# Kernel optimization log

Hardware: AMD Instinct MI355X
Metric: run time of the kernel (lower is better)

Reference implementation:

```python
import jax, jax.numpy as jnp
import numpy as np

D = 1024
N_HEAD = 16
D_HEAD = D // N_HEAD
B, S = 4, 2048
EPS = 1e-6


def rmsnorm(x, w):
    # x: [..., d_head]
    return x / jnp.sqrt(jnp.mean(x * x, axis=-1, keepdims=True) + EPS) * w


def setup_inputs() -> dict:
    key = jax.random.key(0)
    ks = jax.random.split(key, 6)
    x = jax.random.normal(ks[0], (B, S, D), dtype=jnp.float32)
    # causal mask: True means masked (upper triangle above diagonal)
    mask = jnp.triu(jnp.ones((S, S), dtype=bool), k=1)
    scale = 1.0 / np.sqrt(D)
    W_qkv = jax.random.normal(ks[1], (D, 3 * D), dtype=jnp.float32) * scale
    b_qkv = jnp.zeros((3 * D,), dtype=jnp.float32)
    W_o = jax.random.normal(ks[2], (D, D), dtype=jnp.float32) * scale
    b_o = jnp.zeros((D,), dtype=jnp.float32)
    wq = jnp.ones((D_HEAD,), dtype=jnp.float32)
    wk = jnp.ones((D_HEAD,), dtype=jnp.float32)
    return {"x": x, "mask": mask, "W_qkv": W_qkv, "b_qkv": b_qkv,
            "W_o": W_o, "b_o": b_o, "wq": wq, "wk": wk}


def reference(x, mask, W_qkv, b_qkv, W_o, b_o, wq, wk):
    b, s, d = x.shape
    qkv = x @ W_qkv + b_qkv  # [b,s,3d]
    q, k, v = jnp.split(qkv, 3, axis=-1)
    q = q.reshape(b, s, N_HEAD, D_HEAD)
    k = k.reshape(b, s, N_HEAD, D_HEAD)
    v = v.reshape(b, s, N_HEAD, D_HEAD)
    q = rmsnorm(q, wq)
    k = rmsnorm(k, wk)
    # NOTE: no 1/sqrt(d_head) scaling, faithful to the source
    attn = jnp.einsum('bqhd,bkhd->bhqk', q, k)
    attn = jnp.where(mask[None, None, :, :], -jnp.inf, attn)
    attn = jax.nn.softmax(attn, axis=-1)
    z = jnp.einsum('bhqk,bkhd->bqhd', attn, v).reshape(b, s, d)
    return z @ W_o + b_o
```

## Files before the change

kernel.cpp:

```cpp
#include <hip/hip_runtime.h>
#include <cmath>

typedef _Float16 half_t;
typedef _Float16 half8 __attribute__((ext_vector_type(8)));
typedef _Float16 half4v __attribute__((ext_vector_type(4)));
typedef float float4v __attribute__((ext_vector_type(4)));

#define LOG2E 1.44269504088896340736f

#define GLDS16(g, l)                                                                   \
    __builtin_amdgcn_global_load_lds((const __attribute__((address_space(1))) void*)(g), \
                                     (__attribute__((address_space(3))) void*)(l), 16, 0, 0)

#define BAR_LGKM() __asm__ volatile("s_waitcnt lgkmcnt(0)\n\ts_barrier" ::: "memory")
#define BAR_VM(n)  __asm__ volatile("s_waitcnt vmcnt(" #n ")\n\ts_barrier" ::: "memory")

__global__ void cast_f32_f16(const float* __restrict__ in, half_t* __restrict__ out, int n) {
    int i = (blockIdx.x * blockDim.x + threadIdx.x) * 4;
    if (i >= n) return;
    float4 v = *(const float4*)(in + i);
    half4v o;
    o[0] = (half_t)v.x; o[1] = (half_t)v.y; o[2] = (half_t)v.z; o[3] = (half_t)v.w;
    *(half4v*)(out + i) = o;
}

__global__ void transpose_cast(const float* __restrict__ in, half_t* __restrict__ out, int R, int C) {
    __shared__ float tile[32][33];
    int c0 = blockIdx.x * 32, r0 = blockIdx.y * 32;
    int tx = threadIdx.x, ty = threadIdx.y;
    for (int p = 0; p < 4; p++) {
        int r = r0 + ty + p * 8;
        tile[ty + p * 8][tx] = in[(size_t)r * C + c0 + tx];
    }
    __syncthreads();
    for (int p = 0; p < 4; p++) {
        int c = c0 + ty + p * 8;
        out[(size_t)c * R + r0 + tx] = (half_t)tile[tx][ty + p * 8];
    }
}

template <int MODE>
__global__ __launch_bounds__(256, 3) void gemm_f16(
    const half_t* __restrict__ A,
    const half_t* __restrict__ Bt,
    const float* __restrict__ bias,
    void* __restrict__ Cout,
    int M, int N, int K,
    const float* __restrict__ wq, const float* __restrict__ wk,
    half_t* __restrict__ Qh, half_t* __restrict__ Kh)
{
    __shared__ __align__(16) half_t As[3][128 * 32];
    __shared__ __align__(16) half_t Bs[3][128 * 32];
    int t = threadIdx.x;
    int lane = t & 63, w = t >> 6;
    int m0 = blockIdx.x * 128, n0 = blockIdx.y * 128;
    int wm = (w >> 1) * 64, wn = (w & 1) * 64;
    int lrow = lane & 15, quad = lane >> 4;

    int lc = ((t & 3) - (t >> 3)) & 3;
    const half_t* gA = A  + (size_t)(m0 + (t >> 2)) * K + lc * 8;
    const half_t* gB = Bt + (size_t)(n0 + (t >> 2)) * K + lc * 8;
    half_t* ldsA[3] = { &As[0][w * 512], &As[1][w * 512], &As[2][w * 512] };
    half_t* ldsB[3] = { &Bs[0][w * 512], &Bs[1][w * 512], &Bs[2][w * 512] };

    int posq = (quad + (lrow >> 1)) & 3;

    float4v acc[4][4] = {};

    GLDS16(gA,                       ldsA[0]);
    GLDS16(gA + (size_t)64 * K,      ldsA[0] + 2048);
    GLDS16(gB,                       ldsB[0]);
    GLDS16(gB + (size_t)64 * K,      ldsB[0] + 2048);
    GLDS16(gA + 32,                  ldsA[1]);
    GLDS16(gA + (size_t)64 * K + 32, ldsA[1] + 2048);
    GLDS16(gB + 32,                  ldsB[1]);
    GLDS16(gB + (size_t)64 * K + 32, ldsB[1] + 2048);

    int nk = K >> 5;
    for (int ki = 0; ki < nk; ki++) {
        int cur = ki % 3, pre = (ki + 2) % 3;
        BAR_LGKM();
        if (ki + 2 < nk) {
            int kp = (ki + 2) << 5;
            GLDS16(gA + kp,                  ldsA[pre]);
            GLDS16(gA + (size_t)64 * K + kp, ldsA[pre] + 2048);
            GLDS16(gB + kp,                  ldsB[pre]);
            GLDS16(gB + (size_t)64 * K + kp, ldsB[pre] + 2048);
            BAR_VM(8);
        } else if (ki + 1 < nk) {
            BAR_VM(4);
        } else {
            BAR_VM(0);
        }
        half8 af[4], bf[4];
        for (int i = 0; i < 4; i++) af[i] = *(const half8*)(&As[cur][(wm + i * 16 + lrow) * 32 + posq * 8]);
        for (int i = 0; i < 4; i++) bf[i] = *(const half8*)(&Bs[cur][(wn + i * 16 + lrow) * 32 + posq * 8]);
        for (int mi = 0; mi < 4; mi++)
            for (int ni = 0; ni < 4; ni++)
                acc[mi][ni] = __builtin_amdgcn_mfma_f32_16x16x32_f16(af[mi], bf[ni], acc[mi][ni], 0, 0, 0);
    }

    if (MODE == 0) {
        float* out = (float*)Cout;
        for (int mi = 0; mi < 4; mi++)
            for (int ni = 0; ni < 4; ni++)
                for (int r = 0; r < 4; r++) {
                    int gr = m0 + wm + mi * 16 + quad * 4 + r;
                    int gc = n0 + wn + ni * 16 + lrow;
                    out[(size_t)gr * N + gc] = acc[mi][ni][r] + bias[gc];
                }
    } else {
        int nglob = n0 + wn;
        if (nglob < 2048) {
            int isK = nglob >> 10;
            int h = (nglob >> 6) & 15;
            const float* wv = isK ? wk : wq;
            half_t* dst = isK ? Kh : Qh;
            float post = isK ? 1.0f : LOG2E;
            for (int mi = 0; mi < 4; mi++)
                for (int r = 0; r < 4; r++) {
                    int gr = m0 + wm + mi * 16 + quad * 4 + r;
                    float v[4]; float ss = 0.f;
                    for (int ni = 0; ni < 4; ni++) {
                        v[ni] = acc[mi][ni][r] + bias[nglob + ni * 16 + lrow];
                        ss += v[ni] * v[ni];
                    }
                    ss += __shfl_xor(ss, 1);
                    ss += __shfl_xor(ss, 2);
                    ss += __shfl_xor(ss, 4);
                    ss += __shfl_xor(ss, 8);
                    float rr = rsqrtf(ss * (1.0f / 64.0f) + 1e-6f) * post;
                    int bb = gr >> 11, s = gr & 2047;
                    size_t rowbase = ((size_t)((bb * 16 + h) * 2048 + s)) * 64;
                    for (int ni = 0; ni < 4; ni++) {
                        int d = ni * 16 + lrow;
                        dst[rowbase + d] = (half_t)(v[ni] * rr * wv[d]);
                    }
                }
        } else {
            half_t* Vt = (half_t*)Cout;
            for (int mi = 0; mi < 4; mi++) {
                int gr = m0 + wm + mi * 16 + quad * 4;
                int bb = gr >> 11, s = gr & 2047;
                for (int ni = 0; ni < 4; ni++) {
                    int dg = nglob + ni * 16 + lrow - 2048;
                    float bv = bias[nglob + ni * 16 + lrow];
                    half4v oh;
                    for (int r = 0; r < 4; r++) oh[r] = (half_t)(acc[mi][ni][r] + bv);
                    *(half4v*)(Vt + ((size_t)((bb * 16 + (dg >> 6)) * 64 + (dg & 63))) * 2048 + s) = oh;
                }
            }
        }
    }
}

__global__ __launch_bounds__(512, 4) void attn(
    const half_t* __restrict__ Qh, const half_t* __restrict__ Kh, const half_t* __restrict__ Vt,
    half_t* __restrict__ Z)
{
    __shared__ __align__(16) half_t Ks[2][128 * 64];
    __shared__ __align__(16) half_t Vs[2][64 * 128];
    __shared__ __align__(16) half_t Ps[8][16 * 64];

    int bh = blockIdx.x;
    int b = bh >> 4, h = bh & 15;
    int t = threadIdx.x, lane = t & 63, w = t >> 6;
    int lrow = lane & 15, quad = lane >> 4;

    int scc = (lane & 7) ^ ((lane >> 3) & 7);
    const half_t* gK0 = Kh + ((size_t)bh * 2048 + w * 16 + (lane >> 3)) * 64 + scc * 8;
    int vr0 = w * 8 + (lane >> 4);
    int vc0 = (lane & 15) ^ (lane >> 4);
    int vc1 = (lane & 15) ^ ((lane >> 4) + 4);
    const half_t* gV0 = Vt + ((size_t)bh * 64 + vr0) * 2048 + vc0 * 8;
    const half_t* gV1 = Vt + ((size_t)bh * 64 + vr0 + 4) * 2048 + vc1 * 8;
    half_t* ldsK[2] = { &Ks[0][w * 1024], &Ks[1][w * 1024] };
    half_t* ldsV[2] = { &Vs[0][w * 1024], &Vs[1][w * 1024] };

    int sw = lrow & 7;
    int cA = (quad ^ sw) * 8;
    int cB = ((quad + 4) ^ sw) * 8;
    half_t* PsW = &Ps[w][lrow * 64];

    for (int pass = 0; pass < 2; pass++) {
        int qt = pass ? (15 - (int)blockIdx.y) : (int)blockIdx.y;
        int q0w = qt * 128 + w * 16;

        const half_t* Qbase = Qh + ((size_t)bh * 2048 + q0w + lrow) * 64;
        half8 qf0 = *(const half8*)(Qbase + quad * 8);
        half8 qf1 = *(const half8*)(Qbase + 32 + quad * 8);

        float4v ot[4] = {};
        float m = -__builtin_inff(), l = 0.f;

        int nt = qt + 1;
        __syncthreads();
        GLDS16(gK0,       ldsK[0]);
        GLDS16(gK0 + 512, ldsK[0] + 512);
        GLDS16(gV0,       ldsV[0]);
        GLDS16(gV1,       ldsV[0] + 512);

        for (int kt = 0; kt < nt; kt++) {
            int cur = kt & 1, nxt = cur ^ 1;
            int kb = kt * 128;
            BAR_LGKM();
            if (kt + 1 < nt) {
                size_t ko = (size_t)(kb + 128);
                GLDS16(gK0 + ko * 64,       ldsK[nxt]);
                GLDS16(gK0 + ko * 64 + 512, ldsK[nxt] + 512);
                GLDS16(gV0 + ko,            ldsV[nxt]);
                GLDS16(gV1 + ko,            ldsV[nxt] + 512);
                BAR_VM(4);
            } else {
                BAR_VM(0);
            }

            float4v st[8];
            for (int f = 0; f < 8; f++) {
                float4v z = {};
                const half_t* kr = &Ks[cur][(f * 16 + lrow) * 64];
                half8 k0 = *(const half8*)(kr + cA);
                half8 k1 = *(const half8*)(kr + cB);
                z = __builtin_amdgcn_mfma_f32_16x16x32_f16(k0, qf0, z, 0, 0, 0);
                z = __builtin_amdgcn_mfma_f32_16x16x32_f16(k1, qf1, z, 0, 0, 0);
                st[f] = z;
            }
            if (kb + 127 > q0w) {
                int qabs = q0w + lrow;
                for (int f = 0; f < 8; f++)
                    for (int r = 0; r < 4; r++) {
                        int key = kb + f * 16 + quad * 4 + r;
                        if (key > qabs) st[f][r] = -__builtin_inff();
                    }
            }
            float tm = st[0][0];
            for (int f = 0; f < 8; f++)
                for (int r = 0; r < 4; r++) tm = fmaxf(tm, st[f][r]);
            tm = fmaxf(tm, __shfl_xor(tm, 16));
            tm = fmaxf(tm, __shfl_xor(tm, 32));
            float mn = fmaxf(m, tm);
            float alpha = __builtin_amdgcn_exp2f(m - mn);
            m = mn;
            float rs = 0.f;
            uint2 pw1[4];
            for (int f = 0; f < 8; f++) {
                float p0 = __builtin_amdgcn_exp2f(st[f][0] - mn);
                float p1 = __builtin_amdgcn_exp2f(st[f][1] - mn);
                float p2 = __builtin_amdgcn_exp2f(st[f][2] - mn);
                float p3 = __builtin_amdgcn_exp2f(st[f][3] - mn);
                rs += (p0 + p1) + (p2 + p3);
                uint2 pw;
                pw.x = __builtin_bit_cast(unsigned, __builtin_amdgcn_cvt_pkrtz(p0, p1));
                pw.y = __builtin_bit_cast(unsigned, __builtin_amdgcn_cvt_pkrtz(p2, p3));
                if (f < 4) {
                    int cc = (2 * f + (quad >> 1)) ^ sw;
                    *(uint2*)(PsW + cc * 8 + (quad & 1) * 4) = pw;
                } else {
                    pw1[f - 4] = pw;
                }
            }
            rs += __shfl_xor(rs, 16);
            rs += __shfl_xor(rs, 32);
            l = l * alpha + rs;
            for (int f2 = 0; f2 < 4; f2++)
                for (int r = 0; r < 4; r++) ot[f2][r] *= alpha;

            __asm__ volatile("s_waitcnt lgkmcnt(0)" ::: "memory");
            half8 p0v = *(const half8*)(PsW + cA);
            half8 p1v = *(const half8*)(PsW + cB);
            for (int f2 = 0; f2 < 4; f2++) {
                int row = f2 * 16 + lrow;
                half8 v0 = *(const half8*)(&Vs[cur][row * 128 + ((quad ^ sw)) * 8]);
                half8 v1 = *(const half8*)(&Vs[cur][row * 128 + (((4 + quad) ^ sw)) * 8]);
                ot[f2] = __builtin_amdgcn_mfma_f32_16x16x32_f16(v0, p0v, ot[f2], 0, 0, 0);
                ot[f2] = __builtin_amdgcn_mfma_f32_16x16x32_f16(v1, p1v, ot[f2], 0, 0, 0);
            }
            for (int f = 0; f < 4; f++) {
                int cc = (2 * f + (quad >> 1)) ^ sw;
                *(uint2*)(PsW + cc * 8 + (quad & 1) * 4) = pw1[f];
            }
            __asm__ volatile("s_waitcnt lgkmcnt(0)" ::: "memory");
            half8 p2v = *(const half8*)(PsW + cA);
            half8 p3v = *(const half8*)(PsW + cB);
            for (int f2 = 0; f2 < 4; f2++) {
                int row = f2 * 16 + lrow;
                half8 v2 = *(const half8*)(&Vs[cur][row * 128 + (((8 + quad) ^ sw)) * 8]);
                half8 v3 = *(const half8*)(&Vs[cur][row * 128 + (((12 + quad) ^ sw)) * 8]);
                ot[f2] = __builtin_amdgcn_mfma_f32_16x16x32_f16(v2, p2v, ot[f2], 0, 0, 0);
                ot[f2] = __builtin_amdgcn_mfma_f32_16x16x32_f16(v3, p3v, ot[f2], 0, 0, 0);
            }
        }

        float inv = 1.0f / l;
        size_t base = ((size_t)(b * 2048) + q0w + lrow) * 1024 + h * 64;
        for (int f2 = 0; f2 < 4; f2++) {
            half4v oh;
            for (int r = 0; r < 4; r++) oh[r] = (half_t)(ot[f2][r] * inv);
            *(half4v*)(Z + base + f2 * 16 + quad * 4) = oh;
        }
    }
}

extern "C" void kernel_launch(void* const* d_in, const int* in_sizes, int n_in,
                              void* d_out, int out_size, void* d_ws, size_t ws_size,
                              hipStream_t stream)
{
    const float* x     = (const float*)d_in[0];
    const float* W_qkv = (const float*)d_in[2];
    const float* b_qkv = (const float*)d_in[3];
    const float* W_o   = (const float*)d_in[4];
    const float* b_o   = (const float*)d_in[5];
    const float* wq    = (const float*)d_in[6];
    const float* wk    = (const float*)d_in[7];
    float* out = (float*)d_out;

    char* ws = (char*)d_ws;
    half_t* xh   = (half_t*)(ws);
    half_t* Wqt  = (half_t*)(ws + (16ull << 20));
    half_t* Wot  = (half_t*)(ws + (22ull << 20));
    half_t* Qh   = (half_t*)(ws + (40ull << 20));
    half_t* Kh   = (half_t*)(ws + (56ull << 20));
    half_t* Vt   = (half_t*)(ws + (72ull << 20));
    half_t* zh   = xh;

    cast_f32_f16<<<8192, 256, 0, stream>>>(x, xh, 8192 * 1024);
    transpose_cast<<<dim3(96, 32), dim3(32, 8), 0, stream>>>(W_qkv, Wqt, 1024, 3072);
    transpose_cast<<<dim3(32, 32), dim3(32, 8), 0, stream>>>(W_o, Wot, 1024, 1024);
    gemm_f16<1><<<dim3(64, 24), 256, 0, stream>>>(xh, Wqt, b_qkv, Vt, 8192, 3072, 1024,
                                                  wq, wk, Qh, Kh);
    attn<<<dim3(64, 8), 512, 0, stream>>>(Qh, Kh, Vt, zh);
    gemm_f16<0><<<dim3(64, 8), 256, 0, stream>>>(zh, Wot, b_o, out, 8192, 1024, 1024,
                                                 nullptr, nullptr, nullptr, nullptr);
}
```

Baseline: 270.2 us.

## Add 256x256 ping-pong QKV GEMM with XCD-aware block remap and fused RMSNorm epilogue

```diff
diff --git a/kernel.cpp b/kernel.cpp
--- a/kernel.cpp
+++ b/kernel.cpp
@@ -37,6 +37,192 @@
         int c = c0 + ty + p * 8;
         out[(size_t)c * R + r0 + tx] = (half_t)tile[tx][ty + p * 8];
     }
+}
+
+__global__ __launch_bounds__(512, 2) void gemm_qkv(
+    const half_t* __restrict__ A,
+    const half_t* __restrict__ Bt,
+    const float* __restrict__ bias,
+    const float* __restrict__ wq, const float* __restrict__ wk,
+    half_t* __restrict__ Qh, half_t* __restrict__ Kh, half_t* __restrict__ Vt,
+    int M, int N, int K)
+{
+    __shared__ __align__(16) half_t As[2][2][128 * 64];
+    __shared__ __align__(16) half_t Bs[2][2][256 * 32];
+
+    int t = threadIdx.x;
+    int lane = t & 63, w = t >> 6;
+    int lrow = lane & 15, quad = lane >> 4;
+    int wm = w >> 2, wn = w & 3;
+
+    int cpx = gridDim.x >> 3;
+    int bid = blockIdx.x;
+    int wg = (bid & 7) * cpx + (bid >> 3);
+    int nbn = N >> 8;
+    int mb = wg / nbn, nb = wg % nbn;
+    int m0 = mb << 8, n0 = nb << 8;
+
+    int ar = t >> 3;
+    int ac = (t & 7) ^ (ar & 7);
+    const half_t* gAbase = A + (size_t)(m0 + ar) * K + ac * 8;
+    int br = t >> 2;
+    int bc = t & 3;
+    const half_t* gBbase = Bt + (size_t)(n0 + br) * K + bc * 8;
+
+    auto stageA = [&](int buf, int a, int T) {
+        const half_t* s = gAbase + (size_t)a * 128 * K + T * 64;
+        GLDS16(s,                  &As[buf][a][w * 512]);
+        GLDS16(s + (size_t)64 * K, &As[buf][a][4096 + w * 512]);
+    };
+    auto stageB = [&](int buf, int kh, int T) {
+        const half_t* s = gBbase + T * 64 + kh * 32;
+        GLDS16(s,                   &Bs[buf][kh][w * 512]);
+        GLDS16(s + (size_t)128 * K, &Bs[buf][kh][4096 + w * 512]);
+    };
+
+    int sw = lrow & 7;
+    int cx0 = ((0 + quad) ^ sw) * 8;
+    int cx1 = ((4 + quad) ^ sw) * 8;
+    int aoffs = (wm * 64 + lrow) * 64;
+    int boffs = (wn * 64 + lrow) * 32 + quad * 8;
+
+    half8 af[4][2];
+    half8 b0[4], b1[4];
+    float4v acc[2][4][4] = {};
+
+    auto loadA = [&](int buf, int a) {
+        #pragma unroll
+        for (int mi = 0; mi < 4; mi++) {
+            af[mi][0] = *(const half8*)(&As[buf][a][aoffs + mi * 1024 + cx0]);
+            af[mi][1] = *(const half8*)(&As[buf][a][aoffs + mi * 1024 + cx1]);
+        }
+    };
+    auto loadB = [&](int buf, int kh, half8* bf) {
+        #pragma unroll
+        for (int ni = 0; ni < 4; ni++)
+            bf[ni] = *(const half8*)(&Bs[buf][kh][boffs + ni * 512]);
+    };
+
+#define PHASE_OPEN()                                               \
+    do {                                                           \
+        __asm__ volatile("s_barrier" ::: "memory");                \
+        __asm__ volatile("s_waitcnt lgkmcnt(0)" ::: "memory");     \
+        __builtin_amdgcn_sched_barrier(0);                         \
+        __builtin_amdgcn_s_setprio(1);                             \
+    } while (0)
+#define PHASE_CLOSE()                                              \
+    do {                                                           \
+        __builtin_amdgcn_s_setprio(0);                             \
+        __builtin_amdgcn_sched_barrier(0);                         \
+        __asm__ volatile("s_barrier" ::: "memory");                \
+    } while (0)
+#define MFMA16(A_, KH_, BF_)                                                           \
+    do {                                                                               \
+        _Pragma("unroll")                                                              \
+        for (int mi = 0; mi < 4; mi++) {                                               \
+            _Pragma("unroll")                                                          \
+            for (int ni = 0; ni < 4; ni++)                                             \
+                acc[A_][mi][ni] = __builtin_amdgcn_mfma_f32_16x16x32_f16(              \
+                    af[mi][KH_], BF_[ni], acc[A_][mi][ni], 0, 0, 0);                   \
+        }                                                                              \
+    } while (0)
+
+    int nk = K >> 6;
+
+    stageA(0, 0, 0); stageB(0, 0, 0); stageA(0, 1, 0); stageB(0, 1, 0);
+    stageA(1, 0, 1); stageB(1, 0, 1); stageA(1, 1, 1);
+    __asm__ volatile("s_waitcnt vmcnt(6)" ::: "memory");
+    __asm__ volatile("s_barrier" ::: "memory");
+
+    for (int T = 0; T < nk; T++) {
+        int buf = T & 1, nbuf = buf ^ 1;
+        loadA(buf, 0);
+        loadB(buf, 0, b0);
+        if (T + 1 < nk) stageB(nbuf, 1, T + 1);
+        __asm__ volatile("s_waitcnt lgkmcnt(8)" ::: "memory");
+        PHASE_OPEN();
+        MFMA16(0, 0, b0);
+        PHASE_CLOSE();
+        loadB(buf, 1, b1);
+        if (T + 2 < nk) stageA(buf, 0, T + 2);
+        PHASE_OPEN();
+        MFMA16(0, 1, b1);
+        PHASE_CLOSE();
+        loadA(buf, 1);
+        if (T + 2 < nk) stageB(buf, 0, T + 2);
+        PHASE_OPEN();
+        MFMA16(1, 1, b1);
+        PHASE_CLOSE();
+        if (T + 2 < nk) stageA(buf, 1, T + 2);
+        PHASE_OPEN();
+        MFMA16(1, 0, b0);
+        __builtin_amdgcn_s_setprio(0);
+        __builtin_amdgcn_sched_barrier(0);
+        if (T + 2 < nk) {
+            __asm__ volatile("s_waitcnt vmcnt(6)" ::: "memory");
+        } else if (T + 1 < nk) {
+            __asm__ volatile("s_waitcnt vmcnt(0)" ::: "memory");
+        }
+        __asm__ volatile("s_barrier" ::: "memory");
+    }
+
+    int nglob = n0 + wn * 64;
+    if (nglob < 2048) {
+        int isK = nglob >> 10;
+        int h = (nglob >> 6) & 15;
+        const float* wv = isK ? wk : wq;
+        half_t* dst = isK ? Kh : Qh;
+        float post = isK ? 1.0f : LOG2E;
+        #pragma unroll
+        for (int a = 0; a < 2; a++) {
+            #pragma unroll
+            for (int mi = 0; mi < 4; mi++) {
+                #pragma unroll
+                for (int r = 0; r < 4; r++) {
+                    int gr = m0 + a * 128 + wm * 64 + mi * 16 + quad * 4 + r;
+                    float v[4]; float ss = 0.f;
+                    #pragma unroll
+                    for (int ni = 0; ni < 4; ni++) {
+                        v[ni] = acc[a][mi][ni][r] + bias[nglob + ni * 16 + lrow];
+                        ss += v[ni] * v[ni];
+                    }
+                    ss += __shfl_xor(ss, 1);
+                    ss += __shfl_xor(ss, 2);
+                    ss += __shfl_xor(ss, 4);
+                    ss += __shfl_xor(ss, 8);
+                    float rr = rsqrtf(ss * (1.0f / 64.0f) + 1e-6f) * post;
+                    int bb = gr >> 11, s = gr & 2047;
+                    size_t rowbase = ((size_t)((bb * 16 + h) * 2048 + s)) * 64;
+                    #pragma unroll
+                    for (int ni = 0; ni < 4; ni++) {
+                        int d = ni * 16 + lrow;
+                        dst[rowbase + d] = (half_t)(v[ni] * rr * wv[d]);
+                    }
+                }
+            }
+        }
+    } else {
+        #pragma unroll
+        for (int a = 0; a < 2; a++) {
+            #pragma unroll
+            for (int mi = 0; mi < 4; mi++) {
+                int gr = m0 + a * 128 + wm * 64 + mi * 16 + quad * 4;
+                int bb = gr >> 11, s = gr & 2047;
+                #pragma unroll
+                for (int ni = 0; ni < 4; ni++) {
+                    int dg = nglob + ni * 16 + lrow - 2048;
+                    float bv = bias[nglob + ni * 16 + lrow];
+                    half4v oh;
+                    #pragma unroll
+                    for (int r = 0; r < 4; r++) oh[r] = (half_t)(acc[a][mi][ni][r] + bv);
+                    *(half4v*)(Vt + ((size_t)((bb * 16 + (dg >> 6)) * 64 + (dg & 63))) * 2048 + s) = oh;
+                }
+            }
+        }
+    }
+#undef PHASE_OPEN
+#undef PHASE_CLOSE
+#undef MFMA16
 }
 
 template <int MODE>
@@ -326,8 +512,7 @@
     cast_f32_f16<<<8192, 256, 0, stream>>>(x, xh, 8192 * 1024);
     transpose_cast<<<dim3(96, 32), dim3(32, 8), 0, stream>>>(W_qkv, Wqt, 1024, 3072);
     transpose_cast<<<dim3(32, 32), dim3(32, 8), 0, stream>>>(W_o, Wot, 1024, 1024);
-    gemm_f16<1><<<dim3(64, 24), 256, 0, stream>>>(xh, Wqt, b_qkv, Vt, 8192, 3072, 1024,
-                                                  wq, wk, Qh, Kh);
+    gemm_qkv<<<384, 512, 0, stream>>>(xh, Wqt, b_qkv, wq, wk, Qh, Kh, Vt, 8192, 3072, 1024);
     attn<<<dim3(64, 8), 512, 0, stream>>>(Qh, Kh, Vt, zh);
     gemm_f16<0><<<dim3(64, 8), 256, 0, stream>>>(zh, Wot, b_o, out, 8192, 1024, 1024,
                                                  nullptr, nullptr, nullptr, nullptr);
```

Measured after the change: 282.4 us. 1.04x slower.
